# Kernel tuning notes

Hardware: AMD Instinct MI355X
Metric: run time of the kernel (lower is better)

The kernel has to match this reference:

```python
import jax, jax.numpy as jnp
import numpy as np

D = 2048        # input_size / model dim
H = 2816        # hidden_size per expert (GLU -> w1 has 2*H rows)
E = 8           # num_experts
M = 4096        # tokens (batch*seq)


def setup_inputs() -> dict:
    key = jax.random.key(0)
    k1, k2, k3, k4, k5 = jax.random.split(key, 5)
    x = jax.random.normal(k1, (M, D), dtype=jnp.float32)
    # ParallelExperts init: uniform(-1/fan_in_dim, 1/fan_in_dim); scale kept simple here
    w1 = jax.random.uniform(k2, (E, 2 * H, D), dtype=jnp.float32, minval=-1.0, maxval=1.0) / (2 * H)
    w2 = jax.random.uniform(k3, (E, D, H), dtype=jnp.float32, minval=-1.0, maxval=1.0) / D
    router_w = jax.random.normal(k4, (E, D), dtype=jnp.float32) * (1.0 / np.sqrt(D))
    bias = jnp.zeros((D,), dtype=jnp.float32)
    return {"x": x, "w1": w1, "w2": w2, "router_w": router_w, "bias": bias, "top_k": 2}


def _moe_forward(x, w1, w2, router_w, bias, top_k):
    # Router: logits -> softmax (fp32) -> top-k -> renormalize (fused_moe semantics)
    logits = x @ router_w.T                                # [M, E]
    probs = jax.nn.softmax(logits.astype(jnp.float32), axis=-1)
    topk_w, topk_ids = jax.lax.top_k(probs, top_k)         # [M, k]
    topk_w = topk_w / jnp.sum(topk_w, axis=-1, keepdims=True)
    # Dense combine weights [M, E]: gate weight if expert selected, else 0
    m = x.shape[0]
    combine = jnp.zeros((m, w1.shape[0]), dtype=x.dtype)
    combine = combine.at[jnp.arange(m)[:, None], topk_ids].add(topk_w.astype(x.dtype))
    # Grouped expert GEMMs, expressed as a loop over the small fixed expert set.
    # Contribution of expert e is masked by combine[:, e] (zero for unrouted tokens).
    y = jnp.zeros_like(x)
    hdim = w2.shape[2]
    for e in range(w1.shape[0]):
        g = x @ w1[e].T                                    # [M, 2H]
        h = jax.nn.silu(g[:, :hdim]) * g[:, hdim:]          # silu_and_mul (GLU)
        y = y + combine[:, e:e + 1] * (h @ w2[e].T)         # [M, D]
    return y + bias


def reference(x, w1, w2, router_w, bias, top_k):
    return _moe_forward(x, w1, w2, router_w, bias, top_k)
```

## Files before the change

### kernel.cpp

```cpp
#include <hip/hip_runtime.h>
#include <hip/hip_bf16.h>
#include <stdint.h>

#define M_TOK 4096
#define DDIM  2048
#define HDIM  2816
#define NEXP  8
#define PMAX  10240
#define MAXTILES 40
#define NB1   44
#define NB2   16
#define NKT1  32
#define NKT2  44

typedef __attribute__((ext_vector_type(8))) short short8;
typedef __attribute__((ext_vector_type(4))) float f32x4;

#define GLD16(g, l) __builtin_amdgcn_global_load_lds(                              \
    (const __attribute__((address_space(1))) unsigned int*)(g),                    \
    (__attribute__((address_space(3))) unsigned int*)(l), 16, 0, 0)

#define VMCNT(n) asm volatile("s_waitcnt vmcnt(" #n ")" ::: "memory")

__device__ __forceinline__ unsigned short f2bf(float f) {
  unsigned int u = __float_as_uint(f);
  u += 0x7fffu + ((u >> 16) & 1u);
  return (unsigned short)(u >> 16);
}
__device__ __forceinline__ float bf2f(unsigned short u) {
  return __uint_as_float(((unsigned)u) << 16);
}

__global__ void cvt2_bf16_k(const float4* __restrict__ in1, ushort4* __restrict__ out1, int n1,
                            const float4* __restrict__ in2, ushort4* __restrict__ out2, int n2) {
  const int stride = gridDim.x * blockDim.x;
  const int total = n1 + n2;
  int i = blockIdx.x * blockDim.x + threadIdx.x;
  for (; i + stride < total; i += 2 * stride) {
    int ia = i, ib = i + stride;
    float4 va = (ia < n1) ? in1[ia] : in2[ia - n1];
    float4 vb = (ib < n1) ? in1[ib] : in2[ib - n1];
    ushort4 oa, ob;
    oa.x = f2bf(va.x); oa.y = f2bf(va.y); oa.z = f2bf(va.z); oa.w = f2bf(va.w);
    ob.x = f2bf(vb.x); ob.y = f2bf(vb.y); ob.z = f2bf(vb.z); ob.w = f2bf(vb.w);
    if (ia < n1) out1[ia] = oa; else out2[ia - n1] = oa;
    if (ib < n1) out1[ib] = ob; else out2[ib - n1] = ob;
  }
  if (i < total) {
    float4 v = (i < n1) ? in1[i] : in2[i - n1];
    ushort4 o;
    o.x = f2bf(v.x); o.y = f2bf(v.y); o.z = f2bf(v.z); o.w = f2bf(v.w);
    if (i < n1) out1[i] = o; else out2[i - n1] = o;
  }
}

__global__ void init_k(int* __restrict__ tok, int* __restrict__ counts, int* __restrict__ cursors) {
  int i = blockIdx.x * blockDim.x + threadIdx.x;
  if (i < PMAX) tok[i] = -1;
  if (i < NEXP) { counts[i] = 0; cursors[i] = 0; }
}

__global__ __launch_bounds__(256) void router_k(const float4* __restrict__ x4,
                                                const float4* __restrict__ rw4,
                                                ushort4* __restrict__ xb4,
                                                float* __restrict__ wgt,
                                                int* __restrict__ eid,
                                                int* __restrict__ counts) {
  int lane = threadIdx.x & 63;
  int wv = threadIdx.x >> 6;
  int t = blockIdx.x * 4 + wv;
  int base = t * (DDIM / 4);
  float acc[NEXP];
#pragma unroll
  for (int e = 0; e < NEXP; ++e) acc[e] = 0.f;
#pragma unroll
  for (int j = 0; j < DDIM / 4 / 64; ++j) {
    float4 v = x4[base + j * 64 + lane];
    ushort4 o;
    o.x = f2bf(v.x); o.y = f2bf(v.y); o.z = f2bf(v.z); o.w = f2bf(v.w);
    xb4[base + j * 64 + lane] = o;
#pragma unroll
    for (int e = 0; e < NEXP; ++e) {
      float4 w = rw4[e * (DDIM / 4) + j * 64 + lane];
      acc[e] += v.x * w.x + v.y * w.y + v.z * w.z + v.w * w.w;
    }
  }
#pragma unroll
  for (int e = 0; e < NEXP; ++e) {
#pragma unroll
    for (int s = 32; s > 0; s >>= 1) acc[e] += __shfl_xor(acc[e], s, 64);
  }
  if (lane == 0) {
    float mx = acc[0];
#pragma unroll
    for (int e = 1; e < NEXP; ++e) mx = fmaxf(mx, acc[e]);
    float p[NEXP];
#pragma unroll
    for (int e = 0; e < NEXP; ++e) p[e] = expf(acc[e] - mx);
    int e0 = 0; float p0 = p[0];
#pragma unroll
    for (int e = 1; e < NEXP; ++e) if (p[e] > p0) { p0 = p[e]; e0 = e; }
    int e1 = -1; float p1 = -1.f;
#pragma unroll
    for (int e = 0; e < NEXP; ++e) if (e != e0 && p[e] > p1) { p1 = p[e]; e1 = e; }
    float s = p0 + p1;
    wgt[2 * t] = p0 / s; wgt[2 * t + 1] = p1 / s;
    eid[2 * t] = e0;     eid[2 * t + 1] = e1;
    atomicAdd(&counts[e0], 1);
    atomicAdd(&counts[e1], 1);
  }
}

__global__ void offsets_k(const int* __restrict__ counts, int* __restrict__ offs,
                          int* __restrict__ tile2exp, int* __restrict__ tilerow,
                          int* __restrict__ ntiles) {
  if (threadIdx.x == 0 && blockIdx.x == 0) {
    int o = 0, nt = 0;
    for (int e = 0; e < NEXP; ++e) {
      offs[e] = o;
      int c = counts[e];
      int pt = (c + 255) >> 8;
      for (int i = 0; i < pt; ++i) { tile2exp[nt] = e; tilerow[nt] = o + i * 256; ++nt; }
      o += pt << 8;
    }
    offs[NEXP] = o;
    ntiles[0] = nt;
  }
}

__global__ void scatter_k(const int* __restrict__ eid, const int* __restrict__ offs,
                          int* __restrict__ cursors, int* __restrict__ tok,
                          int* __restrict__ slot) {
  int t = blockIdx.x * blockDim.x + threadIdx.x;
  if (t >= M_TOK) return;
#pragma unroll
  for (int k = 0; k < 2; ++k) {
    int e = eid[2 * t + k];
    int p = offs[e] + atomicAdd(&cursors[e], 1);
    tok[p] = t;
    slot[2 * t + k] = p;
  }
}

__global__ __launch_bounds__(256, 2) void gemm1_k(const unsigned short* __restrict__ xb,
                                                  const unsigned short* __restrict__ w1b,
                                                  const int* __restrict__ tok,
                                                  const int* __restrict__ tile2exp,
                                                  const int* __restrict__ tilerow,
                                                  const int* __restrict__ ntiles,
                                                  unsigned short* __restrict__ h) {
  __shared__ char ldsp[65536];
  int mt = blockIdx.x;
  if (mt >= ntiles[0]) return;
  int e = tile2exp[mt], r0 = tilerow[mt];
  int n0 = blockIdx.y * 64;
  int tid = threadIdx.x, lane = tid & 63;
  int wv = tid >> 6, wm = wv >> 1, wn = wv & 1;
  int l15 = lane & 15, lq = lane >> 4;

  int sg = tid & 7, srow = tid >> 3;
  unsigned int aOff[8], bOff[4];
#pragma unroll
  for (int j = 0; j < 8; ++j) {
    int r = j * 32 + srow;
    int t = tok[r0 + r]; if (t < 0) t = 0;
    aOff[j] = (unsigned int)t * (DDIM * 2) + (unsigned int)((sg ^ (r & 7)) << 4);
  }
#pragma unroll
  for (int j = 0; j < 4; ++j) {
    int r = j * 32 + srow;
    int w1row = e * (2 * HDIM) + (r < 64 ? n0 + r : HDIM + n0 + (r - 64));
    bOff[j] = (unsigned int)w1row * (DDIM * 2) + (unsigned int)((sg ^ (r & 7)) << 4);
  }

  int aRd[8], bRd[4];
#pragma unroll
  for (int i = 0; i < 8; ++i) {
    int r = wm * 128 + i * 16 + l15;
    aRd[i] = r * 128 + ((lq ^ (r & 7)) << 4);
  }
#pragma unroll
  for (int i = 0; i < 4; ++i) {
    int r = wn * 64 + i * 16 + l15;
    bRd[i] = r * 128 + ((lq ^ (r & 7)) << 4);
  }

  f32x4 acc[8][4];
#pragma unroll
  for (int mi = 0; mi < 8; ++mi)
#pragma unroll
    for (int ni = 0; ni < 4; ++ni) acc[mi][ni] = (f32x4)(0.f);

  const char* xB = (const char*)xb;
  const char* wB = (const char*)w1b;

#pragma unroll 1
  for (int kt = 0; kt < NKT1; ++kt) {
    __syncthreads();
    unsigned int kb = (unsigned int)kt * 128;
#pragma unroll
    for (int j = 0; j < 8; ++j) GLD16(xB + aOff[j] + kb, ldsp + j * 4096 + tid * 16);
#pragma unroll
    for (int j = 0; j < 4; ++j) GLD16(wB + bOff[j] + kb, ldsp + 32768 + j * 4096 + tid * 16);
    VMCNT(0);
    __syncthreads();
#pragma unroll
    for (int kh = 0; kh < 2; ++kh) {
      int kx = kh << 6;
      short8 a[8], b[4];
#pragma unroll
      for (int i = 0; i < 8; ++i) a[i] = *(const short8*)(ldsp + (aRd[i] ^ kx));
#pragma unroll
      for (int i = 0; i < 4; ++i) b[i] = *(const short8*)(ldsp + 32768 + (bRd[i] ^ kx));
      __builtin_amdgcn_s_setprio(1);
#pragma unroll
      for (int mi = 0; mi < 8; ++mi)
#pragma unroll
        for (int ni = 0; ni < 4; ++ni)
          acc[mi][ni] = __builtin_amdgcn_mfma_f32_16x16x32_bf16(a[mi], b[ni], acc[mi][ni], 0, 0, 0);
      __builtin_amdgcn_s_setprio(0);
    }
  }

  __syncthreads();
  float* xch = (float*)ldsp;
  if (wn == 1) {
#pragma unroll
    for (int mi = 0; mi < 8; ++mi)
#pragma unroll
      for (int ni = 0; ni < 4; ++ni)
#pragma unroll
        for (int j = 0; j < 4; ++j) {
          int r = wm * 128 + mi * 16 + lq * 4 + j;
          int c = ni * 16 + l15;
          xch[r * 64 + (c ^ (lq << 2))] = acc[mi][ni][j];
        }
  }
  __syncthreads();
  if (wn == 0) {
#pragma unroll
    for (int mi = 0; mi < 8; ++mi)
#pragma unroll
      for (int ni = 0; ni < 4; ++ni)
#pragma unroll
        for (int j = 0; j < 4; ++j) {
          int r = wm * 128 + mi * 16 + lq * 4 + j;
          int c = ni * 16 + l15;
          float u = xch[r * 64 + (c ^ (lq << 2))];
          float gg = acc[mi][ni][j];
          float sv = gg / (1.f + expf(-gg));
          h[(size_t)(r0 + r) * HDIM + n0 + c] = f2bf(sv * u);
        }
  }
}

__global__ __launch_bounds__(256, 2) void gemm2_k(const unsigned short* __restrict__ h,
                                                  const unsigned short* __restrict__ w2b,
                                                  const int* __restrict__ tile2exp,
                                                  const int* __restrict__ tilerow,
                                                  const int* __restrict__ ntiles,
                                                  unsigned short* __restrict__ yp) {
  __shared__ char ldsp[49152];
  int mt = blockIdx.x;
  if (mt >= ntiles[0]) return;
  int e = tile2exp[mt], r0 = tilerow[mt];
  int n0 = blockIdx.y * 128;
  int tid = threadIdx.x, lane = tid & 63;
  int wv = tid >> 6, wm = wv >> 1, wn = wv & 1;
  int l15 = lane & 15, lq = lane >> 4;

  int sg = tid & 7, srow = tid >> 3;
  unsigned int aOff[8], bOff[4];
#pragma unroll
  for (int j = 0; j < 8; ++j) {
    int r = j * 32 + srow;
    aOff[j] = (unsigned int)(r0 + r) * (HDIM * 2) + (unsigned int)((sg ^ (r & 7)) << 4);
  }
#pragma unroll
  for (int j = 0; j < 4; ++j) {
    int r = j * 32 + srow;
    bOff[j] = (unsigned int)(e * DDIM + n0 + r) * (HDIM * 2) + (unsigned int)((sg ^ (r & 7)) << 4);
  }

  int aRd[8], bRd[4];
#pragma unroll
  for (int i = 0; i < 8; ++i) {
    int r = wm * 128 + i * 16 + l15;
    aRd[i] = r * 128 + ((lq ^ (r & 7)) << 4);
  }
#pragma unroll
  for (int i = 0; i < 4; ++i) {
    int r = wn * 64 + i * 16 + l15;
    bRd[i] = r * 128 + ((lq ^ (r & 7)) << 4);
  }

  f32x4 acc[8][4];
#pragma unroll
  for (int mi = 0; mi < 8; ++mi)
#pragma unroll
    for (int ni = 0; ni < 4; ++ni) acc[mi][ni] = (f32x4)(0.f);

  const char* hB = (const char*)h;
  const char* wB = (const char*)w2b;

#pragma unroll 1
  for (int kt = 0; kt < NKT2; ++kt) {
    __syncthreads();
    unsigned int kb = (unsigned int)kt * 128;
#pragma unroll
    for (int j = 0; j < 8; ++j) GLD16(hB + aOff[j] + kb, ldsp + j * 4096 + tid * 16);
#pragma unroll
    for (int j = 0; j < 4; ++j) GLD16(wB + bOff[j] + kb, ldsp + 32768 + j * 4096 + tid * 16);
    VMCNT(0);
    __syncthreads();
#pragma unroll
    for (int kh = 0; kh < 2; ++kh) {
      int kx = kh << 6;
      short8 a[8], b[4];
#pragma unroll
      for (int i = 0; i < 8; ++i) a[i] = *(const short8*)(ldsp + (aRd[i] ^ kx));
#pragma unroll
      for (int i = 0; i < 4; ++i) b[i] = *(const short8*)(ldsp + 32768 + (bRd[i] ^ kx));
      __builtin_amdgcn_s_setprio(1);
#pragma unroll
      for (int mi = 0; mi < 8; ++mi)
#pragma unroll
        for (int ni = 0; ni < 4; ++ni)
          acc[mi][ni] = __builtin_amdgcn_mfma_f32_16x16x32_bf16(a[mi], b[ni], acc[mi][ni], 0, 0, 0);
      __builtin_amdgcn_s_setprio(0);
    }
  }

#pragma unroll
  for (int mi = 0; mi < 8; ++mi)
#pragma unroll
    for (int ni = 0; ni < 4; ++ni)
#pragma unroll
      for (int j = 0; j < 4; ++j) {
        int r = r0 + wm * 128 + mi * 16 + lq * 4 + j;
        int c = n0 + wn * 64 + ni * 16 + l15;
        yp[(size_t)r * DDIM + c] = f2bf(acc[mi][ni][j]);
      }
}

__global__ void combine_k(const unsigned short* __restrict__ yp, const float* __restrict__ wgt,
                          const int* __restrict__ slot, const float* __restrict__ bias,
                          float* __restrict__ out) {
  int idx = blockIdx.x * blockDim.x + threadIdx.x;
  int t = idx >> 8, q = (idx & 255) * 8;
  float w0 = wgt[2 * t], w1 = wgt[2 * t + 1];
  int s0 = slot[2 * t], s1 = slot[2 * t + 1];
  short8 a8 = *(const short8*)(yp + (size_t)s0 * DDIM + q);
  short8 b8 = *(const short8*)(yp + (size_t)s1 * DDIM + q);
  float* op = out + (size_t)t * DDIM + q;
#pragma unroll
  for (int k = 0; k < 8; ++k) {
    float av = bf2f((unsigned short)a8[k]);
    float bv = bf2f((unsigned short)b8[k]);
    op[k] = w0 * av + w1 * bv + bias[q + k];
  }
}

extern "C" void kernel_launch(void* const* d_in, const int* in_sizes, int n_in,
                              void* d_out, int out_size, void* d_ws, size_t ws_size,
                              hipStream_t stream) {
  const float* x    = (const float*)d_in[0];
  const float* w1   = (const float*)d_in[1];
  const float* w2   = (const float*)d_in[2];
  const float* rw   = (const float*)d_in[3];
  const float* bias = (const float*)d_in[4];
  float* out = (float*)d_out;

  char* ws = (char*)d_ws;
  size_t off = 0;
  auto alloc = [&](size_t bytes) -> void* {
    void* p = ws + off;
    off = (off + bytes + 255) & ~(size_t)255;
    return p;
  };
  unsigned short* w1b = (unsigned short*)alloc((size_t)NEXP * 2 * HDIM * DDIM * 2);
  unsigned short* w2b = (unsigned short*)alloc((size_t)NEXP * DDIM * HDIM * 2);
  unsigned short* xb  = (unsigned short*)alloc((size_t)M_TOK * DDIM * 2);
  unsigned short* h   = (unsigned short*)alloc((size_t)PMAX * HDIM * 2);
  unsigned short* yp  = (unsigned short*)alloc((size_t)PMAX * DDIM * 2);
  float* wgt          = (float*)alloc((size_t)M_TOK * 2 * 4);
  int* eid            = (int*)alloc((size_t)M_TOK * 2 * 4);
  int* slot           = (int*)alloc((size_t)M_TOK * 2 * 4);
  int* tok            = (int*)alloc((size_t)PMAX * 4);
  int* counts         = (int*)alloc(64 * 4);
  int* cursors        = (int*)alloc(64 * 4);
  int* offs           = (int*)alloc(64 * 4);
  int* ntiles         = (int*)alloc(64 * 4);
  int* tile2exp       = (int*)alloc(128 * 4);
  int* tilerow        = (int*)alloc(128 * 4);

  hipLaunchKernelGGL(init_k, dim3((PMAX + 255) / 256), dim3(256), 0, stream, tok, counts, cursors);
  hipLaunchKernelGGL(cvt2_bf16_k, dim3(4096), dim3(256), 0, stream,
                     (const float4*)w1, (ushort4*)w1b, (int)((size_t)NEXP * 2 * HDIM * DDIM / 4),
                     (const float4*)w2, (ushort4*)w2b, (int)((size_t)NEXP * DDIM * HDIM / 4));
  hipLaunchKernelGGL(router_k, dim3(M_TOK / 4), dim3(256), 0, stream,
                     (const float4*)x, (const float4*)rw, (ushort4*)xb, wgt, eid, counts);
  hipLaunchKernelGGL(offsets_k, dim3(1), dim3(64), 0, stream, counts, offs,
                     tile2exp, tilerow, ntiles);
  hipLaunchKernelGGL(scatter_k, dim3((M_TOK + 255) / 256), dim3(256), 0, stream, eid, offs, cursors, tok, slot);
  hipLaunchKernelGGL(gemm1_k, dim3(MAXTILES, NB1), dim3(256), 0, stream,
                     xb, w1b, tok, tile2exp, tilerow, ntiles, h);
  hipLaunchKernelGGL(gemm2_k, dim3(MAXTILES, NB2), dim3(256), 0, stream,
                     h, w2b, tile2exp, tilerow, ntiles, yp);
  hipLaunchKernelGGL(combine_k, dim3(M_TOK * (DDIM / 8) / 256), dim3(256), 0, stream, yp, wgt, slot, bias, out);
}
```

Before: 765.4 us.

## Widen gemm1 tile to 256x256 with 8 waves and fuse small setup kernels

gemm1 now runs 512 threads (8 waves, 2x4 layout) on a 256-row by 128-gate plus 128-up column tile. Each wave holds matching gate and up accumulators, so SiLU-and-mul happens in registers without the LDS exchange. The N block count is halved. Separately, init_k is folded into the conversion kernel and offsets/scatter are merged into one single-block kernel, removing two launches. The risks are that one block now does all the scatter atomics serially, and the occupancy of 512-thread blocks with 64KB LDS at 2 blocks per CU.

Measured after the change: 839.0 us. 1.1x slower.

```diff
diff --git a/kernel.cpp b/kernel.cpp
--- a/kernel.cpp
+++ b/kernel.cpp
@@ -8,7 +8,7 @@
 #define NEXP  8
 #define PMAX  10240
 #define MAXTILES 40
-#define NB1   44
+#define NB1   22
 #define NB2   16
 #define NKT1  32
 #define NKT2  44
@@ -32,10 +32,15 @@
 }
 
 __global__ void cvt2_bf16_k(const float4* __restrict__ in1, ushort4* __restrict__ out1, int n1,
-                            const float4* __restrict__ in2, ushort4* __restrict__ out2, int n2) {
+                            const float4* __restrict__ in2, ushort4* __restrict__ out2, int n2,
+                            int* __restrict__ tok, int* __restrict__ counts,
+                            int* __restrict__ cursors) {
+  int gid = blockIdx.x * blockDim.x + threadIdx.x;
+  if (gid < PMAX) tok[gid] = -1;
+  if (gid < NEXP) { counts[gid] = 0; cursors[gid] = 0; }
   const int stride = gridDim.x * blockDim.x;
   const int total = n1 + n2;
-  int i = blockIdx.x * blockDim.x + threadIdx.x;
+  int i = gid;
   for (; i + stride < total; i += 2 * stride) {
     int ia = i, ib = i + stride;
     float4 va = (ia < n1) ? in1[ia] : in2[ia - n1];
@@ -52,12 +57,6 @@
     o.x = f2bf(v.x); o.y = f2bf(v.y); o.z = f2bf(v.z); o.w = f2bf(v.w);
     if (i < n1) out1[i] = o; else out2[i - n1] = o;
   }
-}
-
-__global__ void init_k(int* __restrict__ tok, int* __restrict__ counts, int* __restrict__ cursors) {
-  int i = blockIdx.x * blockDim.x + threadIdx.x;
-  if (i < PMAX) tok[i] = -1;
-  if (i < NEXP) { counts[i] = 0; cursors[i] = 0; }
 }
 
 __global__ __launch_bounds__(256) void router_k(const float4* __restrict__ x4,
@@ -111,38 +110,39 @@
   }
 }
 
-__global__ void offsets_k(const int* __restrict__ counts, int* __restrict__ offs,
-                          int* __restrict__ tile2exp, int* __restrict__ tilerow,
-                          int* __restrict__ ntiles) {
-  if (threadIdx.x == 0 && blockIdx.x == 0) {
+__global__ __launch_bounds__(256) void offscat_k(const int* __restrict__ counts,
+                                                 int* __restrict__ tile2exp,
+                                                 int* __restrict__ tilerow,
+                                                 int* __restrict__ ntiles,
+                                                 const int* __restrict__ eid,
+                                                 int* __restrict__ cursors,
+                                                 int* __restrict__ tok,
+                                                 int* __restrict__ slot) {
+  __shared__ int soffs[NEXP];
+  if (threadIdx.x == 0) {
     int o = 0, nt = 0;
     for (int e = 0; e < NEXP; ++e) {
-      offs[e] = o;
+      soffs[e] = o;
       int c = counts[e];
       int pt = (c + 255) >> 8;
       for (int i = 0; i < pt; ++i) { tile2exp[nt] = e; tilerow[nt] = o + i * 256; ++nt; }
       o += pt << 8;
     }
-    offs[NEXP] = o;
     ntiles[0] = nt;
   }
-}
-
-__global__ void scatter_k(const int* __restrict__ eid, const int* __restrict__ offs,
-                          int* __restrict__ cursors, int* __restrict__ tok,
-                          int* __restrict__ slot) {
-  int t = blockIdx.x * blockDim.x + threadIdx.x;
-  if (t >= M_TOK) return;
-#pragma unroll
-  for (int k = 0; k < 2; ++k) {
-    int e = eid[2 * t + k];
-    int p = offs[e] + atomicAdd(&cursors[e], 1);
-    tok[p] = t;
-    slot[2 * t + k] = p;
-  }
-}
-
-__global__ __launch_bounds__(256, 2) void gemm1_k(const unsigned short* __restrict__ xb,
+  __syncthreads();
+  for (int t = threadIdx.x; t < M_TOK; t += 256) {
+#pragma unroll
+    for (int k = 0; k < 2; ++k) {
+      int e = eid[2 * t + k];
+      int p = soffs[e] + atomicAdd(&cursors[e], 1);
+      tok[p] = t;
+      slot[2 * t + k] = p;
+    }
+  }
+}
+
+__global__ __launch_bounds__(512, 2) void gemm1_k(const unsigned short* __restrict__ xb,
                                                   const unsigned short* __restrict__ w1b,
                                                   const int* __restrict__ tok,
                                                   const int* __restrict__ tile2exp,
@@ -153,36 +153,33 @@
   int mt = blockIdx.x;
   if (mt >= ntiles[0]) return;
   int e = tile2exp[mt], r0 = tilerow[mt];
-  int n0 = blockIdx.y * 64;
+  int n0 = blockIdx.y * 128;
   int tid = threadIdx.x, lane = tid & 63;
-  int wv = tid >> 6, wm = wv >> 1, wn = wv & 1;
+  int wv = tid >> 6, wm = wv >> 2, wn = wv & 3;
   int l15 = lane & 15, lq = lane >> 4;
 
-  int sg = tid & 7, srow = tid >> 3;
-  unsigned int aOff[8], bOff[4];
-#pragma unroll
-  for (int j = 0; j < 8; ++j) {
-    int r = j * 32 + srow;
+  int srow = tid >> 3, sq = tid & 7;
+  const char* aSrc[4]; const char* bSrc[4];
+#pragma unroll
+  for (int u = 0; u < 4; ++u) {
+    int r = srow + u * 64;
     int t = tok[r0 + r]; if (t < 0) t = 0;
-    aOff[j] = (unsigned int)t * (DDIM * 2) + (unsigned int)((sg ^ (r & 7)) << 4);
-  }
-#pragma unroll
-  for (int j = 0; j < 4; ++j) {
-    int r = j * 32 + srow;
-    int w1row = e * (2 * HDIM) + (r < 64 ? n0 + r : HDIM + n0 + (r - 64));
-    bOff[j] = (unsigned int)w1row * (DDIM * 2) + (unsigned int)((sg ^ (r & 7)) << 4);
-  }
-
-  int aRd[8], bRd[4];
-#pragma unroll
-  for (int i = 0; i < 8; ++i) {
-    int r = wm * 128 + i * 16 + l15;
-    aRd[i] = r * 128 + ((lq ^ (r & 7)) << 4);
-  }
-#pragma unroll
-  for (int i = 0; i < 4; ++i) {
-    int r = wn * 64 + i * 16 + l15;
-    bRd[i] = r * 128 + ((lq ^ (r & 7)) << 4);
+    aSrc[u] = (const char*)xb + (size_t)t * (DDIM * 2) + ((sq ^ (r & 7)) << 4);
+    int w1row = e * (2 * HDIM) + (r < 128 ? n0 + r : HDIM + n0 + (r - 128));
+    bSrc[u] = (const char*)w1b + (size_t)w1row * (DDIM * 2) + ((sq ^ (r & 7)) << 4);
+  }
+
+  int aoff[8], boff[4];
+#pragma unroll
+  for (int mi = 0; mi < 8; ++mi) {
+    int r = wm * 128 + mi * 16 + l15;
+    aoff[mi] = r * 128 + ((lq ^ (r & 7)) << 4);
+  }
+#pragma unroll
+  for (int ni = 0; ni < 4; ++ni) {
+    int r = (ni < 2) ? (wn * 32 + ni * 16 + l15)
+                     : (128 + wn * 32 + (ni - 2) * 16 + l15);
+    boff[ni] = r * 128 + ((lq ^ (r & 7)) << 4);
   }
 
   f32x4 acc[8][4];
@@ -190,28 +187,26 @@
   for (int mi = 0; mi < 8; ++mi)
 #pragma unroll
     for (int ni = 0; ni < 4; ++ni) acc[mi][ni] = (f32x4)(0.f);
-
-  const char* xB = (const char*)xb;
-  const char* wB = (const char*)w1b;
 
 #pragma unroll 1
   for (int kt = 0; kt < NKT1; ++kt) {
     __syncthreads();
-    unsigned int kb = (unsigned int)kt * 128;
-#pragma unroll
-    for (int j = 0; j < 8; ++j) GLD16(xB + aOff[j] + kb, ldsp + j * 4096 + tid * 16);
-#pragma unroll
-    for (int j = 0; j < 4; ++j) GLD16(wB + bOff[j] + kb, ldsp + 32768 + j * 4096 + tid * 16);
+    size_t kb = (size_t)kt * 128;
+#pragma unroll
+    for (int u = 0; u < 4; ++u) {
+      GLD16(aSrc[u] + kb, ldsp + u * 8192 + tid * 16);
+      GLD16(bSrc[u] + kb, ldsp + 32768 + u * 8192 + tid * 16);
+    }
     VMCNT(0);
     __syncthreads();
 #pragma unroll
-    for (int kh = 0; kh < 2; ++kh) {
-      int kx = kh << 6;
+    for (int s = 0; s < 2; ++s) {
+      int sx = s << 6;
       short8 a[8], b[4];
 #pragma unroll
-      for (int i = 0; i < 8; ++i) a[i] = *(const short8*)(ldsp + (aRd[i] ^ kx));
-#pragma unroll
-      for (int i = 0; i < 4; ++i) b[i] = *(const short8*)(ldsp + 32768 + (bRd[i] ^ kx));
+      for (int i = 0; i < 8; ++i) a[i] = *(const short8*)(ldsp + (aoff[i] ^ sx));
+#pragma unroll
+      for (int i = 0; i < 4; ++i) b[i] = *(const short8*)(ldsp + 32768 + (boff[i] ^ sx));
       __builtin_amdgcn_s_setprio(1);
 #pragma unroll
       for (int mi = 0; mi < 8; ++mi)
@@ -222,36 +217,19 @@
     }
   }
 
-  __syncthreads();
-  float* xch = (float*)ldsp;
-  if (wn == 1) {
-#pragma unroll
-    for (int mi = 0; mi < 8; ++mi)
-#pragma unroll
-      for (int ni = 0; ni < 4; ++ni)
-#pragma unroll
-        for (int j = 0; j < 4; ++j) {
-          int r = wm * 128 + mi * 16 + lq * 4 + j;
-          int c = ni * 16 + l15;
-          xch[r * 64 + (c ^ (lq << 2))] = acc[mi][ni][j];
-        }
-  }
-  __syncthreads();
-  if (wn == 0) {
-#pragma unroll
-    for (int mi = 0; mi < 8; ++mi)
-#pragma unroll
-      for (int ni = 0; ni < 4; ++ni)
-#pragma unroll
-        for (int j = 0; j < 4; ++j) {
-          int r = wm * 128 + mi * 16 + lq * 4 + j;
-          int c = ni * 16 + l15;
-          float u = xch[r * 64 + (c ^ (lq << 2))];
-          float gg = acc[mi][ni][j];
-          float sv = gg / (1.f + expf(-gg));
-          h[(size_t)(r0 + r) * HDIM + n0 + c] = f2bf(sv * u);
-        }
-  }
+#pragma unroll
+  for (int mi = 0; mi < 8; ++mi)
+#pragma unroll
+    for (int ni = 0; ni < 2; ++ni)
+#pragma unroll
+      for (int j = 0; j < 4; ++j) {
+        int r = wm * 128 + mi * 16 + lq * 4 + j;
+        int c = n0 + wn * 32 + ni * 16 + l15;
+        float gg = acc[mi][ni][j];
+        float u = acc[mi][ni + 2][j];
+        float sv = gg / (1.f + expf(-gg));
+        h[(size_t)(r0 + r) * HDIM + c] = f2bf(sv * u);
+      }
 }
 
 __global__ __launch_bounds__(256, 2) void gemm2_k(const unsigned short* __restrict__ h,
@@ -389,21 +367,19 @@
   int* tok            = (int*)alloc((size_t)PMAX * 4);
   int* counts         = (int*)alloc(64 * 4);
   int* cursors        = (int*)alloc(64 * 4);
-  int* offs           = (int*)alloc(64 * 4);
   int* ntiles         = (int*)alloc(64 * 4);
   int* tile2exp       = (int*)alloc(128 * 4);
   int* tilerow        = (int*)alloc(128 * 4);
 
-  hipLaunchKernelGGL(init_k, dim3((PMAX + 255) / 256), dim3(256), 0, stream, tok, counts, cursors);
   hipLaunchKernelGGL(cvt2_bf16_k, dim3(4096), dim3(256), 0, stream,
                      (const float4*)w1, (ushort4*)w1b, (int)((size_t)NEXP * 2 * HDIM * DDIM / 4),
-                     (const float4*)w2, (ushort4*)w2b, (int)((size_t)NEXP * DDIM * HDIM / 4));
+                     (const float4*)w2, (ushort4*)w2b, (int)((size_t)NEXP * DDIM * HDIM / 4),
+                     tok, counts, cursors);
   hipLaunchKernelGGL(router_k, dim3(M_TOK / 4), dim3(256), 0, stream,
                      (const float4*)x, (const float4*)rw, (ushort4*)xb, wgt, eid, counts);
-  hipLaunchKernelGGL(offsets_k, dim3(1), dim3(64), 0, stream, counts, offs,
-                     tile2exp, tilerow, ntiles);
-  hipLaunchKernelGGL(scatter_k, dim3((M_TOK + 255) / 256), dim3(256), 0, stream, eid, offs, cursors, tok, slot);
-  hipLaunchKernelGGL(gemm1_k, dim3(MAXTILES, NB1), dim3(256), 0, stream,
+  hipLaunchKernelGGL(offscat_k, dim3(1), dim3(256), 0, stream,
+                     counts, tile2exp, tilerow, ntiles, eid, cursors, tok, slot);
+  hipLaunchKernelGGL(gemm1_k, dim3(MAXTILES, NB1), dim3(512), 0, stream,
                      xb, w1b, tok, tile2exp, tilerow, ntiles, h);
   hipLaunchKernelGGL(gemm2_k, dim3(MAXTILES, NB2), dim3(256), 0, stream,
                      h, w2b, tile2exp, tilerow, ntiles, yp);
```
